# Optimization experiments

Hardware: AMD Instinct MI355X
Metric: run time of the kernel (lower is better)

The kernel has to match this reference:

```python
import jax, jax.numpy as jnp
import numpy as np

BASE = 257
HASH_MOD = 4096
WINDOWS = (2, 4, 8, 16)
MATCH_OFFSETS = (1, 2, 4, 8)
CHUNK = 32
EPS_LN = 1e-5


def _shift_right(x, k):
    # (B,T) -> shifted right by k along time, zero-filled
    B, T = x.shape
    return jnp.concatenate([jnp.zeros((B, k), x.dtype), x[:, :T - k]], axis=1)


def _rolling_hashes(chars):
    # polynomial rolling hash over each window size, mod HASH_MOD -> (B,T,S) int32
    c = chars.astype(jnp.int32)
    hs = []
    for w in WINDOWS:
        acc = jnp.zeros_like(c)
        p = 1
        for j in range(w):  # small fixed loop (<=16)
            acc = acc + _shift_right(c, j) * p
            p = (p * BASE) % HASH_MOD
        hs.append(acc % HASH_MOD)
    return jnp.stack(hs, axis=2)


def _match_features(chars):
    feats = []
    for k in MATCH_OFFSETS:
        m = (chars == _shift_right(chars, k)).astype(jnp.float32)
        m = m.at[:, :k].set(0.0)
        feats.append(m)
    return jnp.stack(feats, axis=-1)  # (B,T,n_match)


def _layer_norm(x, g, b):
    mu = jnp.mean(x, axis=-1, keepdims=True)
    var = jnp.mean((x - mu) ** 2, axis=-1, keepdims=True)
    return (x - mu) * jax.lax.rsqrt(var + EPS_LN) * g + b


def _forward(chars, emb_byte, hash_tables, Wq, bq, conv_w, conv_b, Win, b_in,
             Wg, bg, Wi, bi, Wo, bo, ln_g, ln_b, mlp_w, mlp_b, Wout, bout):
    B, T = chars.shape
    byte_emb = emb_byte[chars]                       # (B,T,Eb)
    hidx = _rolling_hashes(chars)                    # (B,T,S)
    scale_embeds = jnp.stack(
        [hash_tables[s][hidx[:, :, s]] for s in range(len(WINDOWS))], axis=2
    )                                                # (B,T,S,E)
    # scale attention: query from byte embedding, softmax over scales
    E = scale_embeds.shape[-1]
    q = byte_emb @ Wq + bq                           # (B,T,E)
    scores = jnp.einsum('bte,btse->bts', q, scale_embeds) / jnp.sqrt(jnp.float32(E))
    w = jax.nn.softmax(scores, axis=-1)
    hash_feat = jnp.einsum('bts,btse->bte', w, scale_embeds)
    # causal depthwise conv + silu
    C = hash_feat.shape[-1]
    kk = conv_w.shape[-1]
    ht = jnp.moveaxis(hash_feat, 1, 2)               # (B,C,T)
    ht = jnp.pad(ht, ((0, 0), (0, 0), (kk - 1, 0)))
    ht = jax.lax.conv_general_dilated(
        ht, conv_w, window_strides=(1,), padding='VALID',
        dimension_numbers=('NCH', 'OIH', 'NCH'), feature_group_count=C)
    hash_feat = jax.nn.silu(jnp.moveaxis(ht + conv_b[None, :, None], 2, 1))
    mf = _match_features(chars)
    feat = jnp.concatenate([byte_emb, hash_feat, mf], axis=-1)
    h = jax.nn.silu(feat @ Win + b_in)               # (B,T,H)
    # TinyScan: chunked log-space gated scan, carry across chunks via lax.scan
    gates = jax.nn.sigmoid(h @ Wg + bg)              # (B,T,S)
    drive = (1.0 - gates) * (h @ Wi + bi)
    S = gates.shape[-1]
    nC = T // CHUNK
    g = gates.reshape(B, nC, CHUNK, S).transpose(1, 0, 2, 3)
    d = drive.reshape(B, nC, CHUNK, S).transpose(1, 0, 2, 3)

    def step(hc, ab):
        a, b = ab                                    # (B,K,S)
        log_a = jnp.log(jnp.maximum(a, 1e-6))
        cum_a = jnp.exp(jnp.cumsum(log_a, axis=1))
        inv = 1.0 / jnp.maximum(cum_a, 1e-8)
        cum_wb = jnp.cumsum(b * inv, axis=1)
        out = cum_a * (hc[:, None, :] + cum_wb)
        return out[:, -1], out

    _, states = jax.lax.scan(step, jnp.zeros((B, S), h.dtype), (g, d))
    states = states.transpose(1, 0, 2, 3).reshape(B, T, S)
    h = _layer_norm(h + states @ Wo + bo, ln_g, ln_b)
    # residual MLP blocks: x + silu(Linear(x))
    for l in range(mlp_w.shape[0]):
        h = h + jax.nn.silu(h @ mlp_w[l] + mlp_b[l])
    return h @ Wout + bout                           # (B,T,V)


def setup_inputs() -> dict:
    key = jax.random.key(0)
    ks = jax.random.split(key, 12)
    B, T, V = 8, 8192, 256
    EB, E, H, SS, KC, NM, NR = 64, 64, 512, 32, 4, 4, 3
    feat = EB + E + NM

    def lin(k, i, o):
        return (jax.random.normal(k, (i, o), jnp.float32) / np.sqrt(i)).astype(jnp.float32)

    return {
        'chars': jax.random.randint(ks[0], (B, T), 0, V),
        'emb_byte': jax.random.normal(ks[1], (V, EB), jnp.float32) * 0.02,
        'hash_tables': jax.random.normal(ks[2], (len(WINDOWS), HASH_MOD, E), jnp.float32) * 0.02,
        'Wq': lin(ks[3], EB, E), 'bq': jnp.zeros((E,), jnp.float32),
        'conv_w': jax.random.normal(ks[4], (E, 1, KC), jnp.float32) * 0.2,
        'conv_b': jnp.zeros((E,), jnp.float32),
        'Win': lin(ks[5], feat, H), 'b_in': jnp.zeros((H,), jnp.float32),
        'Wg': lin(ks[6], H, SS), 'bg': jnp.zeros((SS,), jnp.float32),
        'Wi': lin(ks[7], H, SS), 'bi': jnp.zeros((SS,), jnp.float32),
        'Wo': lin(ks[8], SS, H), 'bo': jnp.zeros((H,), jnp.float32),
        'ln_g': jnp.ones((H,), jnp.float32), 'ln_b': jnp.zeros((H,), jnp.float32),
        'mlp_w': jax.random.normal(ks[9], (NR, H, H), jnp.float32) / np.sqrt(H),
        'mlp_b': jnp.zeros((NR, H), jnp.float32),
        'Wout': lin(ks[10], H, V), 'bout': jnp.zeros((V,), jnp.float32),
    }


def reference(chars, emb_byte, hash_tables, Wq, bq, conv_w, conv_b, Win, b_in,
              Wg, bg, Wi, bi, Wo, bo, ln_g, ln_b, mlp_w, mlp_b, Wout, bout):
    return _forward(chars, emb_byte, hash_tables, Wq, bq, conv_w, conv_b, Win, b_in,
                    Wg, bg, Wi, bi, Wo, bo, ln_g, ln_b, mlp_w, mlp_b, Wout, bout)
```

## Files before the change

### kernel.cpp

```cpp
#include <hip/hip_runtime.h>
#include <hip/hip_bf16.h>
#include <math.h>

#define B_ 8
#define T_ 8192
#define V_ 256
#define EB_ 64
#define E_ 64
#define H_ 512
#define SS_ 32
#define FEATP_ 192
#define NCH_ 256
#define CHUNK_ 32

typedef __attribute__((ext_vector_type(8))) short bf8;
typedef __attribute__((ext_vector_type(16))) float accv;

#define AS1(p) (__attribute__((address_space(1))) void*)(void*)(p)
#define AS3(p) (__attribute__((address_space(3))) void*)(void*)(p)

__device__ __forceinline__ float silu_f(float x) { return x / (1.0f + expf(-x)); }
__device__ __forceinline__ float sigm_f(float x) { return 1.0f / (1.0f + expf(-x)); }
__device__ __forceinline__ float bf2f(__hip_bfloat16 v) { return __bfloat162float(v); }
__device__ __forceinline__ __hip_bfloat16 f2bf(float v) { return __float2bfloat16(v); }
__device__ __forceinline__ float us2f(ushort u) {
    union { float f; unsigned int u32; } c; c.u32 = ((unsigned int)u) << 16; return c.f;
}
__device__ __forceinline__ ushort f2us(float v) {
    __hip_bfloat16 t = __float2bfloat16(v);
    return *reinterpret_cast<ushort*>(&t);
}

#define CD_ROW(r, lane) (((r) & 3) + 8 * ((r) >> 2) + 4 * ((lane) >> 5))

__device__ __forceinline__ int xcd_swz(int bid, int nwg) {
    return (bid & 7) * (nwg >> 3) + (bid >> 3);
}

template <int KD>
__device__ __forceinline__ void mm256(const ushort* __restrict__ Ab,
                                      const ushort* __restrict__ Bb,
                                      int m0, int n0, accv (&acc)[4][2]) {
    constexpr int NT = KD / 64;
    __shared__ __align__(1024) ushort lA[32768];
    __shared__ __align__(1024) ushort lB[32768];
    const int tid  = threadIdx.x;
    const int lane = tid & 63;
    const int w    = tid >> 6;
    const int wm   = w >> 2, wn = w & 3;

    const int lrow = lane >> 3;
    const int lcg  = (lane & 7) ^ lrow;
    const ushort* gA = Ab + (size_t)(m0 + w * 32 + lrow) * KD + lcg * 8;
    const ushort* gB = Bb + (size_t)(n0 + w * 32 + lrow) * KD + lcg * 8;
    const int dstw = w * 2048;

    const int swz  = (lane & 7) << 4;
    const int kh16 = (lane >> 5) * 16;
    int oK[4];
#pragma unroll
    for (int ks = 0; ks < 4; ks++) oK[ks] = ((ks * 32 + kh16) ^ swz) >> 1;
    const int rowA = (128 * wm + (lane & 31)) * 64;
    const int rowB = (64 * wn + (lane & 31)) * 64;

#define STG8(slot, kt)                                                                             \
    do {                                                                                           \
        __builtin_amdgcn_global_load_lds(AS1(gA + (kt)),                                           \
                                         AS3(&lA[(slot) * 16384 + dstw + 0 * 512]), 16, 0, 0);     \
        __builtin_amdgcn_global_load_lds(AS1(gB + (kt)),                                           \
                                         AS3(&lB[(slot) * 16384 + dstw + 0 * 512]), 16, 0, 0);     \
        __builtin_amdgcn_global_load_lds(AS1(gA + (size_t)8 * KD + (kt)),                          \
                                         AS3(&lA[(slot) * 16384 + dstw + 1 * 512]), 16, 0, 0);     \
        __builtin_amdgcn_global_load_lds(AS1(gB + (size_t)8 * KD + (kt)),                          \
                                         AS3(&lB[(slot) * 16384 + dstw + 1 * 512]), 16, 0, 0);     \
        __builtin_amdgcn_global_load_lds(AS1(gA + (size_t)16 * KD + (kt)),                         \
                                         AS3(&lA[(slot) * 16384 + dstw + 2 * 512]), 16, 0, 0);     \
        __builtin_amdgcn_global_load_lds(AS1(gB + (size_t)16 * KD + (kt)),                         \
                                         AS3(&lB[(slot) * 16384 + dstw + 2 * 512]), 16, 0, 0);     \
        __builtin_amdgcn_global_load_lds(AS1(gA + (size_t)24 * KD + (kt)),                         \
                                         AS3(&lA[(slot) * 16384 + dstw + 3 * 512]), 16, 0, 0);     \
        __builtin_amdgcn_global_load_lds(AS1(gB + (size_t)24 * KD + (kt)),                         \
                                         AS3(&lB[(slot) * 16384 + dstw + 3 * 512]), 16, 0, 0);     \
    } while (0)

#define PH(slot, ks)                                                                               \
    do {                                                                                           \
        const ushort* pa = &lA[(slot) * 16384 + rowA + oK[ks]];                                    \
        const ushort* pb = &lB[(slot) * 16384 + rowB + oK[ks]];                                    \
        bf8 b0v = *(const bf8*)(pb);                                                               \
        bf8 b1v = *(const bf8*)(pb + 2048);                                                        \
        bf8 a0v = *(const bf8*)(pa);                                                               \
        bf8 a1v = *(const bf8*)(pa + 2048);                                                        \
        bf8 a2v = *(const bf8*)(pa + 4096);                                                        \
        bf8 a3v = *(const bf8*)(pa + 6144);                                                        \
        acc[0][0] = __builtin_amdgcn_mfma_f32_32x32x16_bf16(a0v, b0v, acc[0][0], 0, 0, 0);         \
        acc[0][1] = __builtin_amdgcn_mfma_f32_32x32x16_bf16(a0v, b1v, acc[0][1], 0, 0, 0);         \
        acc[1][0] = __builtin_amdgcn_mfma_f32_32x32x16_bf16(a1v, b0v, acc[1][0], 0, 0, 0);         \
        acc[1][1] = __builtin_amdgcn_mfma_f32_32x32x16_bf16(a1v, b1v, acc[1][1], 0, 0, 0);         \
        acc[2][0] = __builtin_amdgcn_mfma_f32_32x32x16_bf16(a2v, b0v, acc[2][0], 0, 0, 0);         \
        acc[2][1] = __builtin_amdgcn_mfma_f32_32x32x16_bf16(a2v, b1v, acc[2][1], 0, 0, 0);         \
        acc[3][0] = __builtin_amdgcn_mfma_f32_32x32x16_bf16(a3v, b0v, acc[3][0], 0, 0, 0);         \
        acc[3][1] = __builtin_amdgcn_mfma_f32_32x32x16_bf16(a3v, b1v, acc[3][1], 0, 0, 0);         \
    } while (0)

    STG8(0, 0);
#pragma unroll
    for (int t = 0; t < NT - 1; ++t) {
        const int slot = t & 1;
        STG8(slot ^ 1, (t + 1) * 64);
        asm volatile("s_waitcnt vmcnt(8)" ::: "memory");
        __builtin_amdgcn_s_barrier();
        __builtin_amdgcn_sched_barrier(0);
        __builtin_amdgcn_s_setprio(1);
        PH(slot, 0); PH(slot, 1); PH(slot, 2); PH(slot, 3);
        __builtin_amdgcn_s_setprio(0);
        __builtin_amdgcn_s_barrier();
    }
    asm volatile("s_waitcnt vmcnt(0)" ::: "memory");
    __builtin_amdgcn_s_barrier();
    __builtin_amdgcn_sched_barrier(0);
    {
        const int ls = (NT - 1) & 1;
        __builtin_amdgcn_s_setprio(1);
        PH(ls, 0); PH(ls, 1); PH(ls, 2); PH(ls, 3);
        __builtin_amdgcn_s_setprio(0);
    }
#undef STG8
#undef PH
}

__device__ __forceinline__ void zero_acc8(accv (&acc)[4][2]) {
#pragma unroll
    for (int i = 0; i < 4; i++)
#pragma unroll
        for (int j = 0; j < 2; j++)
#pragma unroll
            for (int r = 0; r < 16; r++) acc[i][j][r] = 0.0f;
}

__global__ __launch_bounds__(512, 2) void k_mlp256(const __hip_bfloat16* __restrict__ hin,
                                                   const __hip_bfloat16* __restrict__ Wt,
                                                   const float* __restrict__ bias,
                                                   __hip_bfloat16* __restrict__ hout) {
    accv acc[4][2];
    zero_acc8(acc);
    int wg = xcd_swz(blockIdx.x, 512);
    int m0 = (wg >> 1) * 256, n0 = (wg & 1) * 256;
    int lane = threadIdx.x & 63, w = threadIdx.x >> 6, wm = w >> 2, wn = w & 3;
    mm256<H_>((const ushort*)hin, (const ushort*)Wt, m0, n0, acc);
#pragma unroll
    for (int fr = 0; fr < 4; fr++)
#pragma unroll
        for (int fc = 0; fc < 2; fc++) {
            int col = n0 + 64 * wn + 32 * fc + (lane & 31);
            float bv = bias[col];
#pragma unroll
            for (int r = 0; r < 16; r++) {
                int row = m0 + 128 * wm + 32 * fr + CD_ROW(r, lane);
                float v = acc[fr][fc][r] + bv;
                float res = bf2f(hin[(size_t)row * H_ + col]);
                hout[(size_t)row * H_ + col] = f2bf(res + silu_f(v));
            }
        }
}

__global__ __launch_bounds__(512, 2) void k_win256(const __hip_bfloat16* __restrict__ featb,
                                                   const __hip_bfloat16* __restrict__ Wt,
                                                   const float* __restrict__ bias,
                                                   __hip_bfloat16* __restrict__ hb) {
    accv acc[4][2];
    zero_acc8(acc);
    int wg = xcd_swz(blockIdx.x, 512);
    int m0 = (wg >> 1) * 256, n0 = (wg & 1) * 256;
    int lane = threadIdx.x & 63, w = threadIdx.x >> 6, wm = w >> 2, wn = w & 3;
    mm256<FEATP_>((const ushort*)featb, (const ushort*)Wt, m0, n0, acc);
#pragma unroll
    for (int fr = 0; fr < 4; fr++)
#pragma unroll
        for (int fc = 0; fc < 2; fc++) {
            int col = n0 + 64 * wn + 32 * fc + (lane & 31);
            float bv = bias[col];
#pragma unroll
            for (int r = 0; r < 16; r++) {
                int row = m0 + 128 * wm + 32 * fr + CD_ROW(r, lane);
                hb[(size_t)row * H_ + col] = f2bf(silu_f(acc[fr][fc][r] + bv));
            }
        }
}

__global__ __launch_bounds__(512, 2) void k_out256(const __hip_bfloat16* __restrict__ hb,
                                                   const __hip_bfloat16* __restrict__ Wt,
                                                   const float* __restrict__ bout,
                                                   float* __restrict__ out) {
    accv acc[4][2];
    zero_acc8(acc);
    int wg = xcd_swz(blockIdx.x, 256);
    int m0 = wg * 256;
    int lane = threadIdx.x & 63, w = threadIdx.x >> 6, wm = w >> 2, wn = w & 3;
    mm256<H_>((const ushort*)hb, (const ushort*)Wt, m0, 0, acc);
#pragma unroll
    for (int fr = 0; fr < 4; fr++)
#pragma unroll
        for (int fc = 0; fc < 2; fc++) {
            int col = 64 * wn + 32 * fc + (lane & 31);
            float bv = bout[col];
#pragma unroll
            for (int r = 0; r < 16; r++) {
                int row = m0 + 128 * wm + 32 * fr + CD_ROW(r, lane);
                out[(size_t)row * V_ + col] = acc[fr][fc][r] + bv;
            }
        }
}

template <int KD>
__device__ __forceinline__ void mm128(const __hip_bfloat16* __restrict__ A,
                                      const __hip_bfloat16* __restrict__ Wt,
                                      int m0, int n0, accv (&acc)[2][2]) {
    __shared__ __align__(16) ushort lA[128 * 32];
    __shared__ __align__(16) ushort lB[128 * 32];
    int tid = threadIdx.x;
    int lane = tid & 63, w = tid >> 6;
    int wm = w & 1, wn = w >> 1;
    int c0 = w * 128 + lane;
    int c1 = c0 + 64;
    const ushort* Ab = (const ushort*)A;
    const ushort* Bb = (const ushort*)Wt;
    const ushort* gA0 = Ab + (size_t)(m0 + (c0 >> 2)) * KD + (c0 & 3) * 8;
    const ushort* gA1 = Ab + (size_t)(m0 + (c1 >> 2)) * KD + (c1 & 3) * 8;
    const ushort* gB0 = Bb + (size_t)(n0 + (c0 >> 2)) * KD + (c0 & 3) * 8;
    const ushort* gB1 = Bb + (size_t)(n0 + (c1 >> 2)) * KD + (c1 & 3) * 8;
    ushort* dA0 = &lA[(w * 128) * 8];
    ushort* dA1 = &lA[(w * 128 + 64) * 8];
    ushort* dB0 = &lB[(w * 128) * 8];
    ushort* dB1 = &lB[(w * 128 + 64) * 8];
    const ushort* pa = &lA[(64 * wm + (lane & 31)) * 32 + (lane >> 5) * 8];
    const ushort* pb = &lB[(64 * wn + (lane & 31)) * 32 + (lane >> 5) * 8];

    for (int kt = 0; kt < KD; kt += 32) {
        __builtin_amdgcn_global_load_lds(AS1(gA0 + kt), AS3(dA0), 16, 0, 0);
        __builtin_amdgcn_global_load_lds(AS1(gA1 + kt), AS3(dA1), 16, 0, 0);
        __builtin_amdgcn_global_load_lds(AS1(gB0 + kt), AS3(dB0), 16, 0, 0);
        __builtin_amdgcn_global_load_lds(AS1(gB1 + kt), AS3(dB1), 16, 0, 0);
        __syncthreads();
#pragma unroll
        for (int ks = 0; ks < 2; ks++) {
            bf8 a0 = *(const bf8*)(pa + ks * 16);
            bf8 a1 = *(const bf8*)(pa + 32 * 32 + ks * 16);
            bf8 b0 = *(const bf8*)(pb + ks * 16);
            bf8 b1 = *(const bf8*)(pb + 32 * 32 + ks * 16);
            acc[0][0] = __builtin_amdgcn_mfma_f32_32x32x16_bf16(a0, b0, acc[0][0], 0, 0, 0);
            acc[0][1] = __builtin_amdgcn_mfma_f32_32x32x16_bf16(a0, b1, acc[0][1], 0, 0, 0);
            acc[1][0] = __builtin_amdgcn_mfma_f32_32x32x16_bf16(a1, b0, acc[1][0], 0, 0, 0);
            acc[1][1] = __builtin_amdgcn_mfma_f32_32x32x16_bf16(a1, b1, acc[1][1], 0, 0, 0);
        }
        __syncthreads();
    }
}

__device__ __forceinline__ void zero_acc(accv (&acc)[2][2]) {
#pragma unroll
    for (int i = 0; i < 2; i++)
#pragma unroll
        for (int j = 0; j < 2; j++)
#pragma unroll
            for (int r = 0; r < 16; r++) acc[i][j][r] = 0.0f;
}

__global__ __launch_bounds__(256) void k_womm(const __hip_bfloat16* __restrict__ states_bf,
                                              const __hip_bfloat16* __restrict__ Wt_wo,
                                              const float* __restrict__ bo,
                                              const __hip_bfloat16* __restrict__ hb,
                                              __hip_bfloat16* __restrict__ tmp) {
    accv acc[2][2];
    zero_acc(acc);
    int lane = threadIdx.x & 63, w = threadIdx.x >> 6, wm = w & 1, wn = w >> 1;
    int m0 = blockIdx.x * 128, n0 = blockIdx.y * 128;
    mm128<SS_>(states_bf, Wt_wo, m0, n0, acc);
#pragma unroll
    for (int i = 0; i < 2; i++)
#pragma unroll
        for (int j = 0; j < 2; j++) {
            int col = n0 + 64 * wn + 32 * j + (lane & 31);
            float bv = bo[col];
#pragma unroll
            for (int r = 0; r < 16; r++) {
                int row = m0 + 64 * wm + 32 * i + CD_ROW(r, lane);
                float res = bf2f(hb[(size_t)row * H_ + col]);
                tmp[(size_t)row * H_ + col] = f2bf(res + acc[i][j][r] + bv);
            }
        }
}

__global__ __launch_bounds__(256) void k_ln(const __hip_bfloat16* __restrict__ tmp,
                                            const float* __restrict__ ln_g,
                                            const float* __restrict__ ln_b,
                                            __hip_bfloat16* __restrict__ hb) {
    int wave = threadIdx.x >> 6, lane = threadIdx.x & 63;
    int token = blockIdx.x * 4 + wave;
    const ushort* row = (const ushort*)(tmp + (size_t)token * H_) + lane * 8;
    bf8 xv = *(const bf8*)row;
    float x[8];
    float sm = 0.f, sq = 0.f;
#pragma unroll
    for (int i = 0; i < 8; i++) {
        x[i] = us2f((ushort)xv[i]);
        sm += x[i];
        sq += x[i] * x[i];
    }
#pragma unroll
    for (int off = 32; off; off >>= 1) {
        sm += __shfl_xor(sm, off, 64);
        sq += __shfl_xor(sq, off, 64);
    }
    float mu = sm * (1.0f / 512.0f);
    float var = sq * (1.0f / 512.0f) - mu * mu;
    float rstd = rsqrtf(fmaxf(var, 0.0f) + 1e-5f);
    float4 g0 = *(const float4*)(ln_g + lane * 8);
    float4 g1 = *(const float4*)(ln_g + lane * 8 + 4);
    float4 b0 = *(const float4*)(ln_b + lane * 8);
    float4 b1 = *(const float4*)(ln_b + lane * 8 + 4);
    float gg[8] = {g0.x, g0.y, g0.z, g0.w, g1.x, g1.y, g1.z, g1.w};
    float bb[8] = {b0.x, b0.y, b0.z, b0.w, b1.x, b1.y, b1.z, b1.w};
    bf8 o;
#pragma unroll
    for (int i = 0; i < 8; i++) o[i] = (short)f2us((x[i] - mu) * rstd * gg[i] + bb[i]);
    *(bf8*)((ushort*)(hb + (size_t)token * H_) + lane * 8) = o;
}

__global__ __launch_bounds__(256) void k_gates_mfma(const __hip_bfloat16* __restrict__ hb,
                                                    const __hip_bfloat16* __restrict__ Wt_gd,
                                                    const float* __restrict__ bg,
                                                    const float* __restrict__ bi,
                                                    float* __restrict__ gates,
                                                    float* __restrict__ drive) {
    __shared__ __align__(16) ushort lA[256 * 32];
    __shared__ __align__(16) ushort lB[64 * 32];
    int tid = threadIdx.x, lane = tid & 63, w = tid >> 6;
    int m0 = blockIdx.x * 256;
    accv acc[2][2];
    zero_acc(acc);
    const ushort* Ab = (const ushort*)hb;
    const ushort* Bb = (const ushort*)Wt_gd;
    const ushort* pa = &lA[(64 * w + (lane & 31)) * 32 + (lane >> 5) * 8];
    const ushort* pb = &lB[((lane & 31)) * 32 + (lane >> 5) * 8];
    int cb = w * 64 + lane;
    const ushort* gB = Bb + (size_t)(cb >> 2) * H_ + (cb & 3) * 8;
    for (int kt = 0; kt < H_; kt += 32) {
#pragma unroll
        for (int j = 0; j < 4; j++) {
            int c = w * 256 + j * 64 + lane;
            __builtin_amdgcn_global_load_lds(
                AS1(Ab + (size_t)(m0 + (c >> 2)) * H_ + (c & 3) * 8 + kt),
                AS3(&lA[(w * 256 + j * 64) * 8]), 16, 0, 0);
        }
        __builtin_amdgcn_global_load_lds(AS1(gB + kt), AS3(&lB[(w * 64) * 8]), 16, 0, 0);
        __syncthreads();
#pragma unroll
        for (int ks = 0; ks < 2; ks++) {
            bf8 a0 = *(const bf8*)(pa + ks * 16);
            bf8 a1 = *(const bf8*)(pa + 32 * 32 + ks * 16);
            bf8 b0 = *(const bf8*)(pb + ks * 16);
            bf8 b1 = *(const bf8*)(pb + 32 * 32 + ks * 16);
            acc[0][0] = __builtin_amdgcn_mfma_f32_32x32x16_bf16(a0, b0, acc[0][0], 0, 0, 0);
            acc[0][1] = __builtin_amdgcn_mfma_f32_32x32x16_bf16(a0, b1, acc[0][1], 0, 0, 0);
            acc[1][0] = __builtin_amdgcn_mfma_f32_32x32x16_bf16(a1, b0, acc[1][0], 0, 0, 0);
            acc[1][1] = __builtin_amdgcn_mfma_f32_32x32x16_bf16(a1, b1, acc[1][1], 0, 0, 0);
        }
        __syncthreads();
    }
    int c = lane & 31;
    float bgv = bg[c], biv = bi[c];
#pragma unroll
    for (int i = 0; i < 2; i++)
#pragma unroll
        for (int r = 0; r < 16; r++) {
            int row = m0 + 64 * w + 32 * i + CD_ROW(r, lane);
            float g = sigm_f(acc[i][0][r] + bgv);
            float d = (1.0f - g) * (acc[i][1][r] + biv);
            gates[(size_t)row * SS_ + c] = g;
            drive[(size_t)row * SS_ + c] = d;
        }
}

__global__ __launch_bounds__(256) void k_prep_w(const float* __restrict__ mlp_w,
                                                const float* __restrict__ Wout,
                                                const float* __restrict__ Win,
                                                const float* __restrict__ Wg,
                                                const float* __restrict__ Wi,
                                                const float* __restrict__ Wo,
                                                const float* __restrict__ Wq,
                                                const float* __restrict__ bq,
                                                const float* __restrict__ emb_byte,
                                                __hip_bfloat16* __restrict__ Wt_mlp,
                                                __hip_bfloat16* __restrict__ Wt_out,
                                                __hip_bfloat16* __restrict__ Wt_win,
                                                __hip_bfloat16* __restrict__ Wt_gd,
                                                __hip_bfloat16* __restrict__ Wt_wo,
                                                float* __restrict__ Qtab) {
    int idx = blockIdx.x * 256 + threadIdx.x;
    if (idx < 786432) {
        int l = idx >> 18, rem = idx & 262143;
        int n = rem >> 9, k = rem & 511;
        Wt_mlp[idx] = f2bf(mlp_w[l * 262144 + k * 512 + n]);
    } else if (idx < 917504) {
        int rem = idx - 786432;
        int n = rem >> 9, k = rem & 511;
        Wt_out[rem] = f2bf(Wout[k * 256 + n]);
    } else if (idx < 1015808) {
        int rem = idx - 917504;
        int n = rem / FEATP_, k = rem % FEATP_;
        Wt_win[rem] = f2bf(k < 132 ? Win[k * 512 + n] : 0.0f);
    } else if (idx < 1048576) {
        int rem = idx - 1015808;
        int n = rem >> 9, k = rem & 511;
        Wt_gd[rem] = f2bf(n < 32 ? Wg[k * 32 + n] : Wi[k * 32 + (n - 32)]);
    } else if (idx < 1064960) {
        int rem = idx - 1048576;
        int n = rem >> 5, k = rem & 31;
        Wt_wo[rem] = f2bf(Wo[k * H_ + n]);
    } else if (idx < 1081344) {
        int rem = idx - 1064960;
        int c = rem >> 6, e = rem & 63;
        float a = bq[e];
#pragma unroll 8
        for (int k = 0; k < 64; k++) a += emb_byte[c * 64 + k] * Wq[k * 64 + e];
        Qtab[rem] = a * 0.125f;
    }
}

__global__ __launch_bounds__(256) void k_token_feats(
    const int* __restrict__ chars, const float* __restrict__ emb_byte,
    const float* __restrict__ hash_tables, const float* __restrict__ Qtab,
    __hip_bfloat16* __restrict__ featb, float* __restrict__ hfpre) {
    int wave = threadIdx.x >> 6, lane = threadIdx.x & 63;
    int token = blockIdx.x * 4 + wave;
    int t = token & (T_ - 1);
    int b = token >> 13;
    const int* crow = chars + b * T_;
    int cv[16];
#pragma unroll
    for (int j = 0; j < 16; j++) cv[j] = (t >= j) ? crow[t - j] : 0;
    int acc = 0;
    int hidx[4];
#pragma unroll
    for (int j = 0; j < 16; j++) {
        acc += cv[j] * (1 + 256 * j);
        if (j == 1) hidx[0] = acc & 4095;
        if (j == 3) hidx[1] = acc & 4095;
        if (j == 7) hidx[2] = acc & 4095;
        if (j == 15) hidx[3] = acc & 4095;
    }
    int c0 = cv[0];
    float be = emb_byte[c0 * EB_ + lane];
    float q = Qtab[c0 * 64 + lane];
    float se[4];
#pragma unroll
    for (int s = 0; s < 4; s++) se[s] = hash_tables[(s * 4096 + hidx[s]) * E_ + lane];
    float sc[4];
#pragma unroll
    for (int s = 0; s < 4; s++) {
        float v = q * se[s];
#pragma unroll
        for (int off = 32; off; off >>= 1) v += __shfl_xor(v, off, 64);
        sc[s] = v;
    }
    float mx = fmaxf(fmaxf(sc[0], sc[1]), fmaxf(sc[2], sc[3]));
    float w0 = expf(sc[0] - mx), w1 = expf(sc[1] - mx), w2 = expf(sc[2] - mx), w3 = expf(sc[3] - mx);
    float inv = 1.0f / (w0 + w1 + w2 + w3);
    float hf = (w0 * se[0] + w1 * se[1] + w2 * se[2] + w3 * se[3]) * inv;
    featb[(size_t)token * FEATP_ + lane] = f2bf(be);
    hfpre[(size_t)token * E_ + lane] = hf;
    if (lane < 32) {
        float m = 0.0f;
        if (lane < 4) {
            int k = 1 << lane;
            m = (t >= k && c0 == cv[k]) ? 1.0f : 0.0f;
        }
        featb[(size_t)token * FEATP_ + 128 + lane] = f2bf(m);
    } else {
        featb[(size_t)token * FEATP_ + 128 + lane] = f2bf(0.0f);
    }
}

__global__ __launch_bounds__(256) void k_conv(
    const float* __restrict__ hfpre, const float* __restrict__ conv_w,
    const float* __restrict__ conv_b, __hip_bfloat16* __restrict__ featb) {
    int idx = blockIdx.x * 256 + threadIdx.x;
    int e = idx & 63;
    int bt = idx >> 6;
    int t = bt & (T_ - 1);
    float acc = conv_b[e];
#pragma unroll
    for (int k = 0; k < 4; k++) {
        int tt = t - 3 + k;
        if (tt >= 0) acc += hfpre[(size_t)(bt - 3 + k) * E_ + e] * conv_w[e * 4 + k];
    }
    featb[(size_t)bt * FEATP_ + 64 + e] = f2bf(silu_f(acc));
}

__global__ __launch_bounds__(256) void k_chunk_ab(
    const float* __restrict__ gates, const float* __restrict__ drive,
    float* __restrict__ chA, float* __restrict__ chB) {
    int gid = blockIdx.x * 256 + threadIdx.x;
    int s = gid & 31;
    int n = (gid >> 5) & (NCH_ - 1);
    int b = gid >> 13;
    int base = (b * T_ + n * CHUNK_) * SS_ + s;
    float suml = 0.f, cum_wb = 0.f, cum_a = 1.f;
    for (int i = 0; i < CHUNK_; i++) {
        float g = gates[base + i * SS_];
        float d = drive[base + i * SS_];
        suml += logf(fmaxf(g, 1e-6f));
        cum_a = expf(suml);
        cum_wb += d / fmaxf(cum_a, 1e-8f);
    }
    chA[gid] = cum_a;
    chB[gid] = cum_a * cum_wb;
}

__global__ void k_chunk_scan(const float* __restrict__ chA, const float* __restrict__ chB,
                             float* __restrict__ chH) {
    int tid = threadIdx.x;
    int b = tid >> 5, s = tid & 31;
    const float* pA = chA + (size_t)b * NCH_ * SS_ + s;
    const float* pB = chB + (size_t)b * NCH_ * SS_ + s;
    float* pH = chH + (size_t)b * NCH_ * SS_ + s;
    float hc = 0.f;
    for (int n = 0; n < NCH_; n += 8) {
        float a[8], bb[8];
#pragma unroll
        for (int i = 0; i < 8; i++) {
            a[i] = pA[(n + i) * SS_];
            bb[i] = pB[(n + i) * SS_];
        }
#pragma unroll
        for (int i = 0; i < 8; i++) {
            pH[(n + i) * SS_] = hc;
            hc = a[i] * hc + bb[i];
        }
    }
}

__global__ __launch_bounds__(256) void k_states(
    const float* __restrict__ gates, const float* __restrict__ drive,
    const float* __restrict__ chH, __hip_bfloat16* __restrict__ states_bf) {
    int gid = blockIdx.x * 256 + threadIdx.x;
    int s = gid & 31;
    int n = (gid >> 5) & (NCH_ - 1);
    int b = gid >> 13;
    int base = (b * T_ + n * CHUNK_) * SS_ + s;
    float hc = chH[gid];
    float suml = 0.f, cum_wb = 0.f;
    for (int i = 0; i < CHUNK_; i++) {
        float g = gates[base + i * SS_];
        float d = drive[base + i * SS_];
        suml += logf(fmaxf(g, 1e-6f));
        float cum_a = expf(suml);
        cum_wb += d / fmaxf(cum_a, 1e-8f);
        states_bf[base + i * SS_] = f2bf(cum_a * (hc + cum_wb));
    }
}

extern "C" void kernel_launch(void* const* d_in, const int* in_sizes, int n_in,
                              void* d_out, int out_size, void* d_ws, size_t ws_size,
                              hipStream_t stream) {
    (void)in_sizes; (void)n_in; (void)out_size; (void)ws_size;
    const int*   chars       = (const int*)  d_in[0];
    const float* emb_byte    = (const float*)d_in[1];
    const float* hash_tables = (const float*)d_in[2];
    const float* Wq          = (const float*)d_in[3];
    const float* bq          = (const float*)d_in[4];
    const float* conv_w      = (const float*)d_in[5];
    const float* conv_b      = (const float*)d_in[6];
    const float* Win         = (const float*)d_in[7];
    const float* b_in        = (const float*)d_in[8];
    const float* Wg          = (const float*)d_in[9];
    const float* bg          = (const float*)d_in[10];
    const float* Wi          = (const float*)d_in[11];
    const float* bi          = (const float*)d_in[12];
    const float* Wo          = (const float*)d_in[13];
    const float* bo          = (const float*)d_in[14];
    const float* ln_g        = (const float*)d_in[15];
    const float* ln_b        = (const float*)d_in[16];
    const float* mlp_w       = (const float*)d_in[17];
    const float* mlp_b       = (const float*)d_in[18];
    const float* Wout        = (const float*)d_in[19];
    const float* bout        = (const float*)d_in[20];
    float* out = (float*)d_out;

    const size_t NTOK = (size_t)B_ * T_;
    char* p = (char*)d_ws;
    auto alloc = [&](size_t bytes) { void* r = (void*)p; p += (bytes + 255) & ~(size_t)255; return r; };
    __hip_bfloat16* featb = (__hip_bfloat16*)alloc(NTOK * FEATP_ * 2);
    float*          hfpre = (float*)alloc(NTOK * E_ * 4);
    __hip_bfloat16* hbA   = (__hip_bfloat16*)alloc(NTOK * H_ * 2);
    __hip_bfloat16* hbB   = (__hip_bfloat16*)alloc(NTOK * H_ * 2);
    float*          gates = (float*)alloc(NTOK * SS_ * 4);
    float*          drive = (float*)alloc(NTOK * SS_ * 4);
    __hip_bfloat16* states_bf = (__hip_bfloat16*)alloc(NTOK * SS_ * 2);
    float*          chA   = (float*)alloc((size_t)B_ * NCH_ * SS_ * 4);
    float*          chB   = (float*)alloc((size_t)B_ * NCH_ * SS_ * 4);
    float*          chH   = (float*)alloc((size_t)B_ * NCH_ * SS_ * 4);
    __hip_bfloat16* Wt_mlp= (__hip_bfloat16*)alloc(3 * 512 * 512 * 2);
    __hip_bfloat16* Wt_out= (__hip_bfloat16*)alloc(256 * 512 * 2);
    __hip_bfloat16* Wt_win= (__hip_bfloat16*)alloc(512 * FEATP_ * 2);
    __hip_bfloat16* Wt_gd = (__hip_bfloat16*)alloc(64 * 512 * 2);
    __hip_bfloat16* Wt_wo = (__hip_bfloat16*)alloc(512 * SS_ * 2);
    float*          Qtab  = (float*)alloc(256 * 64 * 4);

    k_prep_w<<<4224, 256, 0, stream>>>(mlp_w, Wout, Win, Wg, Wi, Wo, Wq, bq, emb_byte,
                                       Wt_mlp, Wt_out, Wt_win, Wt_gd, Wt_wo, Qtab);
    k_token_feats<<<NTOK / 4, 256, 0, stream>>>(chars, emb_byte, hash_tables, Qtab, featb, hfpre);
    k_conv<<<NTOK * E_ / 256, 256, 0, stream>>>(hfpre, conv_w, conv_b, featb);
    k_win256<<<512, 512, 0, stream>>>(featb, Wt_win, b_in, hbA);
    k_gates_mfma<<<NTOK / 256, 256, 0, stream>>>(hbA, Wt_gd, bg, bi, gates, drive);
    k_chunk_ab<<<B_ * NCH_ * SS_ / 256, 256, 0, stream>>>(gates, drive, chA, chB);
    k_chunk_scan<<<1, 256, 0, stream>>>(chA, chB, chH);
    k_states<<<B_ * NCH_ * SS_ / 256, 256, 0, stream>>>(gates, drive, chH, states_bf);
    k_womm<<<dim3(NTOK / 128, 4), 256, 0, stream>>>(states_bf, Wt_wo, bo, hbA, hbB);
    k_ln<<<NTOK / 4, 256, 0, stream>>>(hbB, ln_g, ln_b, hbA);
    k_mlp256<<<512, 512, 0, stream>>>(hbA, Wt_mlp, mlp_b, hbB);
    k_mlp256<<<512, 512, 0, stream>>>(hbB, Wt_mlp + 262144, mlp_b + 512, hbA);
    k_mlp256<<<512, 512, 0, stream>>>(hbA, Wt_mlp + 524288, mlp_b + 1024, hbB);
    k_out256<<<256, 512, 0, stream>>>(hbB, Wt_out, bout, out);
}
```

Measured before the change: 521.2 us.

## Fuse Wo projection, layernorm, three MLP layers and output GEMM into one LDS-resident kernel

Replaces six kernel launches (Wo matmul plus residual, layernorm, three residual MLP layers, output projection) with a single kernel. Each block keeps a 128-row slab of the hidden state (128x512 bf16, 128KB) in swizzled LDS across all stages and streams weight K-slices through a small LDS buffer, with a register prefetch of the next slice. This removes the global round-trips of the 8 MB hidden activations between stages and the launch gaps. The cost is one block per CU with about 160KB of LDS, tiles of only 128 rows, and two barriers per K-step. The weights are re-read by every block, which leaves less latency hiding than the earlier 256x256 tiled GEMMs.

```diff
diff --git a/kernel.cpp b/kernel.cpp
--- a/kernel.cpp
+++ b/kernel.cpp
@@ -138,32 +138,6 @@
             for (int r = 0; r < 16; r++) acc[i][j][r] = 0.0f;
 }
 
-__global__ __launch_bounds__(512, 2) void k_mlp256(const __hip_bfloat16* __restrict__ hin,
-                                                   const __hip_bfloat16* __restrict__ Wt,
-                                                   const float* __restrict__ bias,
-                                                   __hip_bfloat16* __restrict__ hout) {
-    accv acc[4][2];
-    zero_acc8(acc);
-    int wg = xcd_swz(blockIdx.x, 512);
-    int m0 = (wg >> 1) * 256, n0 = (wg & 1) * 256;
-    int lane = threadIdx.x & 63, w = threadIdx.x >> 6, wm = w >> 2, wn = w & 3;
-    mm256<H_>((const ushort*)hin, (const ushort*)Wt, m0, n0, acc);
-#pragma unroll
-    for (int fr = 0; fr < 4; fr++)
-#pragma unroll
-        for (int fc = 0; fc < 2; fc++) {
-            int col = n0 + 64 * wn + 32 * fc + (lane & 31);
-            float bv = bias[col];
-#pragma unroll
-            for (int r = 0; r < 16; r++) {
-                int row = m0 + 128 * wm + 32 * fr + CD_ROW(r, lane);
-                float v = acc[fr][fc][r] + bv;
-                float res = bf2f(hin[(size_t)row * H_ + col]);
-                hout[(size_t)row * H_ + col] = f2bf(res + silu_f(v));
-            }
-        }
-}
-
 __global__ __launch_bounds__(512, 2) void k_win256(const __hip_bfloat16* __restrict__ featb,
                                                    const __hip_bfloat16* __restrict__ Wt,
                                                    const float* __restrict__ bias,
@@ -188,143 +162,294 @@
         }
 }
 
-__global__ __launch_bounds__(512, 2) void k_out256(const __hip_bfloat16* __restrict__ hb,
-                                                   const __hip_bfloat16* __restrict__ Wt,
-                                                   const float* __restrict__ bout,
-                                                   float* __restrict__ out) {
-    accv acc[4][2];
-    zero_acc8(acc);
-    int wg = xcd_swz(blockIdx.x, 256);
-    int m0 = wg * 256;
-    int lane = threadIdx.x & 63, w = threadIdx.x >> 6, wm = w >> 2, wn = w & 3;
-    mm256<H_>((const ushort*)hb, (const ushort*)Wt, m0, 0, acc);
-#pragma unroll
-    for (int fr = 0; fr < 4; fr++)
-#pragma unroll
-        for (int fc = 0; fc < 2; fc++) {
-            int col = 64 * wn + 32 * fc + (lane & 31);
-            float bv = bout[col];
-#pragma unroll
-            for (int r = 0; r < 16; r++) {
-                int row = m0 + 128 * wm + 32 * fr + CD_ROW(r, lane);
-                out[(size_t)row * V_ + col] = acc[fr][fc][r] + bv;
-            }
-        }
-}
-
-template <int KD>
-__device__ __forceinline__ void mm128(const __hip_bfloat16* __restrict__ A,
-                                      const __hip_bfloat16* __restrict__ Wt,
-                                      int m0, int n0, accv (&acc)[2][2]) {
-    __shared__ __align__(16) ushort lA[128 * 32];
-    __shared__ __align__(16) ushort lB[128 * 32];
-    int tid = threadIdx.x;
-    int lane = tid & 63, w = tid >> 6;
-    int wm = w & 1, wn = w >> 1;
-    int c0 = w * 128 + lane;
-    int c1 = c0 + 64;
-    const ushort* Ab = (const ushort*)A;
-    const ushort* Bb = (const ushort*)Wt;
-    const ushort* gA0 = Ab + (size_t)(m0 + (c0 >> 2)) * KD + (c0 & 3) * 8;
-    const ushort* gA1 = Ab + (size_t)(m0 + (c1 >> 2)) * KD + (c1 & 3) * 8;
-    const ushort* gB0 = Bb + (size_t)(n0 + (c0 >> 2)) * KD + (c0 & 3) * 8;
-    const ushort* gB1 = Bb + (size_t)(n0 + (c1 >> 2)) * KD + (c1 & 3) * 8;
-    ushort* dA0 = &lA[(w * 128) * 8];
-    ushort* dA1 = &lA[(w * 128 + 64) * 8];
-    ushort* dB0 = &lB[(w * 128) * 8];
-    ushort* dB1 = &lB[(w * 128 + 64) * 8];
-    const ushort* pa = &lA[(64 * wm + (lane & 31)) * 32 + (lane >> 5) * 8];
-    const ushort* pb = &lB[(64 * wn + (lane & 31)) * 32 + (lane >> 5) * 8];
-
-    for (int kt = 0; kt < KD; kt += 32) {
-        __builtin_amdgcn_global_load_lds(AS1(gA0 + kt), AS3(dA0), 16, 0, 0);
-        __builtin_amdgcn_global_load_lds(AS1(gA1 + kt), AS3(dA1), 16, 0, 0);
-        __builtin_amdgcn_global_load_lds(AS1(gB0 + kt), AS3(dB0), 16, 0, 0);
-        __builtin_amdgcn_global_load_lds(AS1(gB1 + kt), AS3(dB1), 16, 0, 0);
-        __syncthreads();
-#pragma unroll
-        for (int ks = 0; ks < 2; ks++) {
-            bf8 a0 = *(const bf8*)(pa + ks * 16);
-            bf8 a1 = *(const bf8*)(pa + 32 * 32 + ks * 16);
-            bf8 b0 = *(const bf8*)(pb + ks * 16);
-            bf8 b1 = *(const bf8*)(pb + 32 * 32 + ks * 16);
-            acc[0][0] = __builtin_amdgcn_mfma_f32_32x32x16_bf16(a0, b0, acc[0][0], 0, 0, 0);
-            acc[0][1] = __builtin_amdgcn_mfma_f32_32x32x16_bf16(a0, b1, acc[0][1], 0, 0, 0);
-            acc[1][0] = __builtin_amdgcn_mfma_f32_32x32x16_bf16(a1, b0, acc[1][0], 0, 0, 0);
-            acc[1][1] = __builtin_amdgcn_mfma_f32_32x32x16_bf16(a1, b1, acc[1][1], 0, 0, 0);
-        }
-        __syncthreads();
-    }
-}
-
-__device__ __forceinline__ void zero_acc(accv (&acc)[2][2]) {
-#pragma unroll
-    for (int i = 0; i < 2; i++)
-#pragma unroll
-        for (int j = 0; j < 2; j++)
-#pragma unroll
-            for (int r = 0; r < 16; r++) acc[i][j][r] = 0.0f;
-}
-
-__global__ __launch_bounds__(256) void k_womm(const __hip_bfloat16* __restrict__ states_bf,
-                                              const __hip_bfloat16* __restrict__ Wt_wo,
-                                              const float* __restrict__ bo,
-                                              const __hip_bfloat16* __restrict__ hb,
-                                              __hip_bfloat16* __restrict__ tmp) {
-    accv acc[2][2];
-    zero_acc(acc);
-    int lane = threadIdx.x & 63, w = threadIdx.x >> 6, wm = w & 1, wn = w >> 1;
-    int m0 = blockIdx.x * 128, n0 = blockIdx.y * 128;
-    mm128<SS_>(states_bf, Wt_wo, m0, n0, acc);
-#pragma unroll
-    for (int i = 0; i < 2; i++)
-#pragma unroll
-        for (int j = 0; j < 2; j++) {
-            int col = n0 + 64 * wn + 32 * j + (lane & 31);
-            float bv = bo[col];
-#pragma unroll
-            for (int r = 0; r < 16; r++) {
-                int row = m0 + 64 * wm + 32 * i + CD_ROW(r, lane);
-                float res = bf2f(hb[(size_t)row * H_ + col]);
-                tmp[(size_t)row * H_ + col] = f2bf(res + acc[i][j][r] + bv);
-            }
-        }
-}
-
-__global__ __launch_bounds__(256) void k_ln(const __hip_bfloat16* __restrict__ tmp,
-                                            const float* __restrict__ ln_g,
-                                            const float* __restrict__ ln_b,
-                                            __hip_bfloat16* __restrict__ hb) {
-    int wave = threadIdx.x >> 6, lane = threadIdx.x & 63;
-    int token = blockIdx.x * 4 + wave;
-    const ushort* row = (const ushort*)(tmp + (size_t)token * H_) + lane * 8;
-    bf8 xv = *(const bf8*)row;
-    float x[8];
-    float sm = 0.f, sq = 0.f;
-#pragma unroll
-    for (int i = 0; i < 8; i++) {
-        x[i] = us2f((ushort)xv[i]);
-        sm += x[i];
-        sq += x[i] * x[i];
-    }
-#pragma unroll
-    for (int off = 32; off; off >>= 1) {
-        sm += __shfl_xor(sm, off, 64);
-        sq += __shfl_xor(sq, off, 64);
-    }
-    float mu = sm * (1.0f / 512.0f);
-    float var = sq * (1.0f / 512.0f) - mu * mu;
-    float rstd = rsqrtf(fmaxf(var, 0.0f) + 1e-5f);
-    float4 g0 = *(const float4*)(ln_g + lane * 8);
-    float4 g1 = *(const float4*)(ln_g + lane * 8 + 4);
-    float4 b0 = *(const float4*)(ln_b + lane * 8);
-    float4 b1 = *(const float4*)(ln_b + lane * 8 + 4);
-    float gg[8] = {g0.x, g0.y, g0.z, g0.w, g1.x, g1.y, g1.z, g1.w};
-    float bb[8] = {b0.x, b0.y, b0.z, b0.w, b1.x, b1.y, b1.z, b1.w};
-    bf8 o;
-#pragma unroll
-    for (int i = 0; i < 8; i++) o[i] = (short)f2us((x[i] - mu) * rstd * gg[i] + bb[i]);
-    *(bf8*)((ushort*)(hb + (size_t)token * H_) + lane * 8) = o;
+__global__ __launch_bounds__(512, 1) void k_tail(
+    const __hip_bfloat16* __restrict__ states_bf,
+    const __hip_bfloat16* __restrict__ Wt_wo,
+    const float* __restrict__ bo,
+    const __hip_bfloat16* __restrict__ h_in,
+    const float* __restrict__ ln_g,
+    const float* __restrict__ ln_b,
+    const __hip_bfloat16* __restrict__ Wt_mlp,
+    const float* __restrict__ mlp_b,
+    const __hip_bfloat16* __restrict__ Wt_out,
+    const float* __restrict__ bout,
+    float* __restrict__ out) {
+    __shared__ __align__(1024) ushort hA[65536];
+    __shared__ __align__(1024) ushort lW[16384];
+    const int tid = threadIdx.x, lane = tid & 63, w = tid >> 6;
+    const int wm = w >> 2, wn = w & 3;
+    const int l31 = lane & 31, lh = lane >> 5;
+    const int m0 = xcd_swz(blockIdx.x, 512) * 128;
+
+    accv acc[2][4];
+#pragma unroll
+    for (int i = 0; i < 2; ++i)
+#pragma unroll
+        for (int j = 0; j < 4; ++j)
+#pragma unroll
+            for (int r = 0; r < 16; ++r) acc[i][j][r] = 0.0f;
+
+    {
+        const ushort* Wo_u = (const ushort*)Wt_wo;
+#pragma unroll
+        for (int l = 0; l < 4; ++l) {
+            int rbase = w * 64 + l * 16;
+            const ushort* src = Wo_u + (size_t)(rbase + (lane >> 2)) * 32
+                                + (((lane & 3) ^ ((lane >> 3) & 3)) << 3);
+            __builtin_amdgcn_global_load_lds(AS1(src), AS3(&lW[rbase * 32]), 16, 0, 0);
+        }
+    }
+    const ushort* Sp = (const ushort*)states_bf + (size_t)(m0 + wm * 64 + l31) * 32 + lh * 8;
+    bf8 s00 = *(const bf8*)(Sp);
+    bf8 s01 = *(const bf8*)(Sp + 16);
+    bf8 s10 = *(const bf8*)(Sp + 1024);
+    bf8 s11 = *(const bf8*)(Sp + 1024 + 16);
+    {
+        const ushort* hsrc = (const ushort*)h_in + (size_t)m0 * 512;
+#pragma unroll
+        for (int i = 0; i < 16; ++i) {
+            int row = w * 16 + i;
+            const ushort* src = hsrc + (size_t)row * 512
+                                + (((lane & 56) | ((lane & 7) ^ (i & 7))) << 3);
+            __builtin_amdgcn_global_load_lds(AS1(src), AS3(&hA[row * 512]), 16, 0, 0);
+        }
+    }
+    asm volatile("s_waitcnt vmcnt(16)" ::: "memory");
+    asm volatile("s_waitcnt lgkmcnt(0)" ::: "memory");
+    __builtin_amdgcn_s_barrier();
+    __builtin_amdgcn_sched_barrier(0);
+
+#pragma unroll
+    for (int ks = 0; ks < 2; ++ks) {
+#pragma unroll
+        for (int fc = 0; fc < 4; ++fc) {
+            int nr = wn * 128 + fc * 32 + l31;
+            int c2 = (ks * 2 + lh) ^ ((nr >> 1) & 3);
+            bf8 bv_ = *(const bf8*)&lW[nr * 32 + c2 * 8];
+            acc[0][fc] = __builtin_amdgcn_mfma_f32_32x32x16_bf16(ks == 0 ? s00 : s01, bv_,
+                                                                 acc[0][fc], 0, 0, 0);
+            acc[1][fc] = __builtin_amdgcn_mfma_f32_32x32x16_bf16(ks == 0 ? s10 : s11, bv_,
+                                                                 acc[1][fc], 0, 0, 0);
+        }
+    }
+    asm volatile("s_waitcnt vmcnt(0)" ::: "memory");
+    asm volatile("s_waitcnt lgkmcnt(0)" ::: "memory");
+    __builtin_amdgcn_s_barrier();
+    __builtin_amdgcn_sched_barrier(0);
+    {
+        float bov[4];
+#pragma unroll
+        for (int fc = 0; fc < 4; ++fc) bov[fc] = bo[wn * 128 + fc * 32 + l31];
+#pragma unroll
+        for (int fr = 0; fr < 2; ++fr)
+#pragma unroll
+            for (int fc = 0; fc < 4; ++fc) {
+                int c = wn * 128 + fc * 32 + l31;
+                int ch = c >> 3;
+#pragma unroll
+                for (int r = 0; r < 16; ++r) {
+                    int rl = wm * 64 + fr * 32 + CD_ROW(r, lane);
+                    int idx = rl * 512 + (((ch & 56) | ((ch & 7) ^ (rl & 7))) << 3) + (c & 7);
+                    hA[idx] = f2us(us2f(hA[idx]) + acc[fr][fc][r] + bov[fc]);
+                }
+            }
+    }
+    asm volatile("s_waitcnt lgkmcnt(0)" ::: "memory");
+    __builtin_amdgcn_s_barrier();
+
+    {
+        float4 g0 = *(const float4*)(ln_g + lane * 8);
+        float4 g1 = *(const float4*)(ln_g + lane * 8 + 4);
+        float4 b0 = *(const float4*)(ln_b + lane * 8);
+        float4 b1 = *(const float4*)(ln_b + lane * 8 + 4);
+        float gg[8] = {g0.x, g0.y, g0.z, g0.w, g1.x, g1.y, g1.z, g1.w};
+        float bb[8] = {b0.x, b0.y, b0.z, b0.w, b1.x, b1.y, b1.z, b1.w};
+        for (int i = 0; i < 16; ++i) {
+            int row = w * 16 + i;
+            int sw = (lane & 56) | ((lane & 7) ^ (row & 7));
+            ushort* prow = &hA[row * 512 + sw * 8];
+            bf8 xv = *(const bf8*)prow;
+            float x[8];
+            float sm = 0.f, sq = 0.f;
+#pragma unroll
+            for (int j = 0; j < 8; ++j) {
+                x[j] = us2f((ushort)xv[j]);
+                sm += x[j];
+                sq += x[j] * x[j];
+            }
+#pragma unroll
+            for (int off = 32; off; off >>= 1) {
+                sm += __shfl_xor(sm, off, 64);
+                sq += __shfl_xor(sq, off, 64);
+            }
+            float mu = sm * (1.0f / 512.0f);
+            float var = sq * (1.0f / 512.0f) - mu * mu;
+            float rstd = rsqrtf(fmaxf(var, 0.0f) + 1e-5f);
+            bf8 o;
+#pragma unroll
+            for (int j = 0; j < 8; ++j)
+                o[j] = (short)f2us((x[j] - mu) * rstd * gg[j] + bb[j]);
+            *(bf8*)prow = o;
+        }
+    }
+    asm volatile("s_waitcnt lgkmcnt(0)" ::: "memory");
+    __builtin_amdgcn_s_barrier();
+
+    for (int layer = 0; layer < 3; ++layer) {
+        const ushort* Wl = (const ushort*)Wt_mlp + (size_t)layer * 262144;
+        const float* bl = mlp_b + layer * 512;
+        float blv[4];
+#pragma unroll
+        for (int fc = 0; fc < 4; ++fc) blv[fc] = bl[wn * 128 + fc * 32 + l31];
+#pragma unroll
+        for (int i = 0; i < 2; ++i)
+#pragma unroll
+            for (int j = 0; j < 4; ++j)
+#pragma unroll
+                for (int r = 0; r < 16; ++r) acc[i][j][r] = 0.0f;
+        {
+            const ushort* ws = Wl + (size_t)tid * 512;
+            bf8 w0 = *(const bf8*)(ws);
+            bf8 w1 = *(const bf8*)(ws + 8);
+            bf8 w2 = *(const bf8*)(ws + 16);
+            bf8 w3 = *(const bf8*)(ws + 24);
+            ushort* wd = &lW[tid * 32];
+            int x = (tid >> 1) & 3;
+            *(bf8*)&wd[(0 ^ x) * 8] = w0;
+            *(bf8*)&wd[(1 ^ x) * 8] = w1;
+            *(bf8*)&wd[(2 ^ x) * 8] = w2;
+            *(bf8*)&wd[(3 ^ x) * 8] = w3;
+        }
+        asm volatile("s_waitcnt lgkmcnt(0)" ::: "memory");
+        __builtin_amdgcn_s_barrier();
+        for (int s = 0; s < 16; ++s) {
+            bf8 n0, n1, n2, n3;
+            if (s < 15) {
+                const ushort* ws = Wl + (size_t)tid * 512 + (s + 1) * 32;
+                n0 = *(const bf8*)(ws);
+                n1 = *(const bf8*)(ws + 8);
+                n2 = *(const bf8*)(ws + 16);
+                n3 = *(const bf8*)(ws + 24);
+            }
+            __builtin_amdgcn_s_setprio(1);
+#pragma unroll
+            for (int ks = 0; ks < 2; ++ks) {
+                int ch = s * 4 + ks * 2 + lh;
+                int sw = (ch & 56) | ((ch & 7) ^ (lane & 7));
+                bf8 a0 = *(const bf8*)&hA[(wm * 64 + l31) * 512 + sw * 8];
+                bf8 a1 = *(const bf8*)&hA[(wm * 64 + 32 + l31) * 512 + sw * 8];
+#pragma unroll
+                for (int fc = 0; fc < 4; ++fc) {
+                    int nr = wn * 128 + fc * 32 + l31;
+                    int c2 = (ks * 2 + lh) ^ ((nr >> 1) & 3);
+                    bf8 bfv = *(const bf8*)&lW[nr * 32 + c2 * 8];
+                    acc[0][fc] = __builtin_amdgcn_mfma_f32_32x32x16_bf16(a0, bfv, acc[0][fc], 0, 0, 0);
+                    acc[1][fc] = __builtin_amdgcn_mfma_f32_32x32x16_bf16(a1, bfv, acc[1][fc], 0, 0, 0);
+                }
+            }
+            __builtin_amdgcn_s_setprio(0);
+            asm volatile("s_waitcnt lgkmcnt(0)" ::: "memory");
+            __builtin_amdgcn_s_barrier();
+            if (s < 15) {
+                ushort* wd = &lW[tid * 32];
+                int x = (tid >> 1) & 3;
+                *(bf8*)&wd[(0 ^ x) * 8] = n0;
+                *(bf8*)&wd[(1 ^ x) * 8] = n1;
+                *(bf8*)&wd[(2 ^ x) * 8] = n2;
+                *(bf8*)&wd[(3 ^ x) * 8] = n3;
+            }
+            asm volatile("s_waitcnt lgkmcnt(0)" ::: "memory");
+            __builtin_amdgcn_s_barrier();
+        }
+#pragma unroll
+        for (int fr = 0; fr < 2; ++fr)
+#pragma unroll
+            for (int fc = 0; fc < 4; ++fc) {
+                int c = wn * 128 + fc * 32 + l31;
+                int ch = c >> 3;
+#pragma unroll
+                for (int r = 0; r < 16; ++r) {
+                    int rl = wm * 64 + fr * 32 + CD_ROW(r, lane);
+                    int idx = rl * 512 + (((ch & 56) | ((ch & 7) ^ (rl & 7))) << 3) + (c & 7);
+                    float hv = us2f(hA[idx]);
+                    hA[idx] = f2us(hv + silu_f(acc[fr][fc][r] + blv[fc]));
+                }
+            }
+        asm volatile("s_waitcnt lgkmcnt(0)" ::: "memory");
+        __builtin_amdgcn_s_barrier();
+    }
+
+    {
+        const ushort* Wl = (const ushort*)Wt_out;
+        float bov2[2];
+        bov2[0] = bout[wn * 64 + l31];
+        bov2[1] = bout[wn * 64 + 32 + l31];
+#pragma unroll
+        for (int i = 0; i < 2; ++i)
+#pragma unroll
+            for (int j = 0; j < 2; ++j)
+#pragma unroll
+                for (int r = 0; r < 16; ++r) acc[i][j][r] = 0.0f;
+        {
+            const ushort* ws = Wl + (size_t)(tid >> 1) * 512 + (tid & 1) * 16;
+            bf8 w0 = *(const bf8*)(ws);
+            bf8 w1 = *(const bf8*)(ws + 8);
+            ushort* wd = &lW[(tid >> 1) * 32];
+            int x = (tid >> 2) & 3;
+            int c0 = (tid & 1) * 2;
+            *(bf8*)&wd[(c0 ^ x) * 8] = w0;
+            *(bf8*)&wd[((c0 + 1) ^ x) * 8] = w1;
+        }
+        asm volatile("s_waitcnt lgkmcnt(0)" ::: "memory");
+        __builtin_amdgcn_s_barrier();
+        for (int s = 0; s < 16; ++s) {
+            bf8 n0, n1;
+            if (s < 15) {
+                const ushort* ws = Wl + (size_t)(tid >> 1) * 512 + (s + 1) * 32 + (tid & 1) * 16;
+                n0 = *(const bf8*)(ws);
+                n1 = *(const bf8*)(ws + 8);
+            }
+            __builtin_amdgcn_s_setprio(1);
+#pragma unroll
+            for (int ks = 0; ks < 2; ++ks) {
+                int ch = s * 4 + ks * 2 + lh;
+                int sw = (ch & 56) | ((ch & 7) ^ (lane & 7));
+                bf8 a0 = *(const bf8*)&hA[(wm * 64 + l31) * 512 + sw * 8];
+                bf8 a1 = *(const bf8*)&hA[(wm * 64 + 32 + l31) * 512 + sw * 8];
+#pragma unroll
+                for (int fc = 0; fc < 2; ++fc) {
+                    int nr = wn * 64 + fc * 32 + l31;
+                    int c2 = (ks * 2 + lh) ^ ((nr >> 1) & 3);
+                    bf8 bfv = *(const bf8*)&lW[nr * 32 + c2 * 8];
+                    acc[0][fc] = __builtin_amdgcn_mfma_f32_32x32x16_bf16(a0, bfv, acc[0][fc], 0, 0, 0);
+                    acc[1][fc] = __builtin_amdgcn_mfma_f32_32x32x16_bf16(a1, bfv, acc[1][fc], 0, 0, 0);
+                }
+            }
+            __builtin_amdgcn_s_setprio(0);
+            asm volatile("s_waitcnt lgkmcnt(0)" ::: "memory");
+            __builtin_amdgcn_s_barrier();
+            if (s < 15) {
+                ushort* wd = &lW[(tid >> 1) * 32];
+                int x = (tid >> 2) & 3;
+                int c0 = (tid & 1) * 2;
+                *(bf8*)&wd[(c0 ^ x) * 8] = n0;
+                *(bf8*)&wd[((c0 + 1) ^ x) * 8] = n1;
+            }
+            asm volatile("s_waitcnt lgkmcnt(0)" ::: "memory");
+            __builtin_amdgcn_s_barrier();
+        }
+#pragma unroll
+        for (int fr = 0; fr < 2; ++fr)
+#pragma unroll
+            for (int fc = 0; fc < 2; ++fc) {
+                int col = wn * 64 + fc * 32 + l31;
+#pragma unroll
+                for (int r = 0; r < 16; ++r) {
+                    int rl = wm * 64 + fr * 32 + CD_ROW(r, lane);
+                    out[(size_t)(m0 + rl) * V_ + col] = acc[fr][fc][r] + bov2[fc];
+                }
+            }
+    }
 }
 
 __global__ __launch_bounds__(256) void k_gates_mfma(const __hip_bfloat16* __restrict__ hb,
@@ -338,7 +463,12 @@
     int tid = threadIdx.x, lane = tid & 63, w = tid >> 6;
     int m0 = blockIdx.x * 256;
     accv acc[2][2];
-    zero_acc(acc);
+#pragma unroll
+    for (int i = 0; i < 2; i++)
+#pragma unroll
+        for (int j = 0; j < 2; j++)
+#pragma unroll
+            for (int r = 0; r < 16; r++) acc[i][j][r] = 0.0f;
     const ushort* Ab = (const ushort*)hb;
     const ushort* Bb = (const ushort*)Wt_gd;
     const ushort* pa = &lA[(64 * w + (lane & 31)) * 32 + (lane >> 5) * 8];
@@ -617,10 +747,7 @@
     k_chunk_ab<<<B_ * NCH_ * SS_ / 256, 256, 0, stream>>>(gates, drive, chA, chB);
     k_chunk_scan<<<1, 256, 0, stream>>>(chA, chB, chH);
     k_states<<<B_ * NCH_ * SS_ / 256, 256, 0, stream>>>(gates, drive, chH, states_bf);
-    k_womm<<<dim3(NTOK / 128, 4), 256, 0, stream>>>(states_bf, Wt_wo, bo, hbA, hbB);
-    k_ln<<<NTOK / 4, 256, 0, stream>>>(hbB, ln_g, ln_b, hbA);
-    k_mlp256<<<512, 512, 0, stream>>>(hbA, Wt_mlp, mlp_b, hbB);
-    k_mlp256<<<512, 512, 0, stream>>>(hbB, Wt_mlp + 262144, mlp_b + 512, hbA);
-    k_mlp256<<<512, 512, 0, stream>>>(hbA, Wt_mlp + 524288, mlp_b + 1024, hbB);
-    k_out256<<<256, 512, 0, stream>>>(hbB, Wt_out, bout, out);
-}
+    k_tail<<<512, 512, 0, stream>>>(states_bf, Wt_wo, bo, hbA, ln_g, ln_b,
+                                    Wt_mlp, mlp_b, Wt_out, bout, out);
+    (void)hbB;
+}
```

New measurement: 524.0 us. No clear change (+0.5%).
